# Performance work log

Measured on AMD Instinct MI355X. Metric: run time of the kernel, lower is better.

Reference implementation:

```python
import jax, jax.numpy as jnp
import numpy as np
from jax import lax

B, C, T = 512, 63, 250          # batch, EEG channels, timepoints
S = 10                           # number of subjects
E = 4                            # emb_size of CNN projection
HID, PROJ = 184, 1024            # hidden_dim (=4*46), embed_dim
EPS = 1e-5
DN = ('NCHW', 'OIHW', 'NCHW')


def setup_inputs() -> dict:
    key = jax.random.key(0)
    ks = jax.random.split(key, 16)
    p = {}
    p['x'] = jax.random.normal(ks[0], (B, C, T), dtype=jnp.float32)
    p['subjects'] = jax.random.randint(ks[1], (B,), 0, S, dtype=jnp.int32)
    # per-subject Linear(T, T): weight [S, T, T], bias [S, T]
    p['W_subj'] = jax.random.normal(ks[2], (S, T, T), dtype=jnp.float32) * 0.02
    p['b_subj'] = jnp.zeros((S, T), dtype=jnp.float32)
    # tsconv
    p['conv1_w'] = jax.random.normal(ks[3], (40, 1, 1, 5), dtype=jnp.float32) * 0.1
    p['conv1_b'] = jnp.zeros((40,), dtype=jnp.float32)
    p['bn1_g'] = jnp.ones((40,), dtype=jnp.float32)
    p['bn1_b'] = jnp.zeros((40,), dtype=jnp.float32)
    p['conv2_w'] = jax.random.normal(ks[4], (40, 40, C, 1), dtype=jnp.float32) * 0.02
    p['conv2_b'] = jnp.zeros((40,), dtype=jnp.float32)
    p['bn2_g'] = jnp.ones((40,), dtype=jnp.float32)
    p['bn2_b'] = jnp.zeros((40,), dtype=jnp.float32)
    # 1x1 projection conv to emb_size
    p['proj_w'] = jax.random.normal(ks[5], (E, 40, 1, 1), dtype=jnp.float32) * 0.1
    p['proj_b'] = jnp.zeros((E,), dtype=jnp.float32)
    # MLP projector
    p['fc1_w'] = jax.random.normal(ks[6], (PROJ, HID), dtype=jnp.float32) * 0.05
    p['fc1_b'] = jnp.zeros((PROJ,), dtype=jnp.float32)
    p['fc2_w'] = jax.random.normal(ks[7], (PROJ, PROJ), dtype=jnp.float32) * 0.02
    p['fc2_b'] = jnp.zeros((PROJ,), dtype=jnp.float32)
    p['ln_g'] = jnp.ones((PROJ,), dtype=jnp.float32)
    p['ln_b'] = jnp.zeros((PROJ,), dtype=jnp.float32)
    return p


def _bn(h, g, b):
    # BatchNorm2d with batch statistics over (N, H, W), NCHW layout
    mu = jnp.mean(h, axis=(0, 2, 3), keepdims=True)
    var = jnp.var(h, axis=(0, 2, 3), keepdims=True)
    return (h - mu) * lax.rsqrt(var + EPS) * g[None, :, None, None] + b[None, :, None, None]


def _avgpool_w(h, k, s):
    # average pool over last (W) dim, kernel k stride s
    summed = lax.reduce_window(h, 0.0, lax.add, (1, 1, 1, k), (1, 1, 1, s), 'VALID')
    return summed / k


def reference(x, subjects, W_subj, b_subj, conv1_w, conv1_b, bn1_g, bn1_b,
              conv2_w, conv2_b, bn2_g, bn2_b, proj_w, proj_b,
              fc1_w, fc1_b, fc2_w, fc2_b, ln_g, ln_b):
    # --- subject-conditioned linear dispatch (grouped GEMM via gather) ---
    Wg = W_subj[subjects]                      # [B, T, T]
    bg = b_subj[subjects]                      # [B, T]
    x_eeg = jnp.einsum('bct,bst->bcs', x, Wg) + bg[:, None, :]   # [B, C, T]

    # --- Spatio_Temporal_CNN ---
    h = x_eeg[:, None, :, :]                   # [B, 1, C, T]
    h = lax.conv_general_dilated(h, conv1_w, (1, 1), 'VALID', dimension_numbers=DN)
    h = h + conv1_b[None, :, None, None]       # [B, 40, C, 246]
    h = _avgpool_w(h, 17, 5)                   # [B, 40, C, 46]
    h = jax.nn.elu(_bn(h, bn1_g, bn1_b))
    h = lax.conv_general_dilated(h, conv2_w, (1, 1), 'VALID', dimension_numbers=DN)
    h = h + conv2_b[None, :, None, None]       # [B, 40, 1, 46]
    h = jax.nn.elu(_bn(h, bn2_g, bn2_b))       # dropout = identity (eval)
    h = lax.conv_general_dilated(h, proj_w, (1, 1), 'VALID', dimension_numbers=DN)
    h = h + proj_b[None, :, None, None]        # [B, E, 1, 46]
    # Rearrange 'b e h w -> b (h w) e' then flatten -> [B, 46*E] = [B, 184]
    z = jnp.transpose(h, (0, 2, 3, 1)).reshape(h.shape[0], -1)

    # --- MLP projector ---
    h1 = z @ fc1_w.T + fc1_b                   # [B, 1024]
    r = jax.nn.gelu(h1, approximate=False) @ fc2_w.T + fc2_b
    h2 = h1 + r                                # ResidualAdd (dropout = identity)
    mu = jnp.mean(h2, axis=-1, keepdims=True)
    var = jnp.var(h2, axis=-1, keepdims=True)
    return (h2 - mu) * lax.rsqrt(var + EPS) * ln_g + ln_b
```

## Files before the change

### kernel.cpp

```cpp
#include <hip/hip_runtime.h>
#include <hip/hip_bf16.h>

#define K2 2520
#define PROJ 1024
#define HID 184
#define N1F (512.f*63.f*46.f)
#define N2F (512.f*46.f)

typedef float f32x4 __attribute__((ext_vector_type(4)));
typedef short bf16x8 __attribute__((ext_vector_type(8)));
typedef unsigned short u16;
typedef unsigned short ushort8 __attribute__((ext_vector_type(8)));
typedef unsigned int u32;
typedef unsigned int u32x4 __attribute__((ext_vector_type(4)));

__device__ __forceinline__ u16 f2bf(float f) {
    unsigned u = __builtin_bit_cast(unsigned, f);
    return (u16)((u + 0x7FFFu + ((u >> 16) & 1u)) >> 16);
}
__device__ __forceinline__ float bf2f(u16 h) {
    unsigned u = ((unsigned)h) << 16;
    return __builtin_bit_cast(float, u);
}
__device__ __forceinline__ u32 cvtpk(float lo, float hi) {
    u32 r;
    asm("v_cvt_pk_bf16_f32 %0, %1, %2" : "=v"(r) : "v"(lo), "v"(hi));
    return r;
}

__global__ void kX(const float* __restrict__ W, const float* __restrict__ w2,
                   const float* __restrict__ fw1, const float* __restrict__ fw2,
                   u16* __restrict__ Wbf, u16* __restrict__ Wbf2,
                   u16* __restrict__ fwbf1, u16* __restrict__ fwbf2, float* stats) {
    int bid = blockIdx.x, tid = threadIdx.x;
    if (bid == 0 && tid < 320) stats[tid] = 0.f;
    if (bid < 2560) {
        int i = bid*256 + tid;
        int j  = i & 7, kg = (i >> 3) & 3, row = (i >> 5) & 15;
        int nf = (i >> 9) & 15, ks = (i >> 13) & 7, sj = i >> 16;
        int s_ = nf*16 + row, t_ = ks*32 + kg*8 + j;
        float v = (s_ < 250 && t_ < 250) ? W[(size_t)sj*62500 + s_*250 + t_] : 0.f;
        Wbf[i] = f2bf(v);
    } else if (bid < 3034) {
        int i = (bid-2560)*256 + tid;
        int n = i / 2528, k = i - n*2528;
        float v = 0.f;
        if (n < 40 && k < K2) { int c = k/40, o = k - c*40; v = w2[n*K2 + o*63 + c]; }
        Wbf2[i] = f2bf(v);
    } else if (bid < 3802) {
        int i = (bid-3034)*256 + tid;
        int n = i/192, k = i - n*192;
        fwbf1[i] = f2bf(k < HID ? fw1[n*HID + k] : 0.f);
    } else {
        int i = (bid-3802)*256 + tid;
        fwbf2[i] = f2bf(fw2[i]);
    }
}

#define XS(c,s) xs[(c)*258 + (s)]
__global__ __launch_bounds__(256) void kAB(const float* __restrict__ x,
                                           const int* __restrict__ subj,
                                           const u16* __restrict__ Wpk,
                                           const float* __restrict__ bsub,
                                           const float* __restrict__ w1,
                                           const float* __restrict__ b1,
                                           u16* __restrict__ pooled,
                                           float* __restrict__ stats) {
    __shared__ float xs[32*258 + 16];
    __shared__ u16 effh[48*32] __attribute__((aligned(16)));
    __shared__ u16 effl[48*32] __attribute__((aligned(16)));
    __shared__ float biasL[256];
    __shared__ float sS[4][48], sQ[4][48];
    int b = blockIdx.x, ch = blockIdx.y;
    int sj = subj[b];
    int tid = threadIdx.x;
    int wv = tid >> 6, lane = tid & 63, row = lane & 15, kg = lane >> 4;

    {
        int srow = tid >> 3, st8 = tid & 7;
        int cg0 = ch*32 + srow;
        const float* xrow = x + ((size_t)b*63 + (cg0 < 63 ? cg0 : 62))*250;
        #pragma unroll
        for (int q = 0; q < 16; ++q) {
            int c2i = st8 + 8*q;
            if (c2i < 125) {
                float2 v = *(const float2*)&xrow[2*c2i];
                *(float2*)&XS(srow, 2*c2i) = v;
            }
        }
        XS(srow, 250 + st8) = 0.f;
        if (tid < 16) xs[32*258 + tid] = 0.f;
    }
    biasL[tid] = (tid < 250) ? bsub[sj*250 + tid] : 0.f;
    for (int i = tid; i < 1536; i += 256) {
        int o = i >> 5, tap = i & 31;
        float e = 0.f;
        if (o < 40 && tap < 21) {
            #pragma unroll
            for (int k = 0; k < 5; ++k) { int u = tap - k; if (u >= 0 && u <= 16) e += w1[o*5+k]; }
            e *= (1.f/17.f);
        }
        u16 h = f2bf(e);
        effh[i] = h;
        effl[i] = f2bf(e - bf2f(h));
    }
    __syncthreads();

    int cgrp = wv & 1, nfh = wv >> 1;
    const u16* Wp = Wpk + (size_t)sj*65536 + ((size_t)row*4 + kg)*8;
    f32x4 acc[8];
    #pragma unroll
    for (int i = 0; i < 8; ++i) acc[i] = (f32x4){0.f,0.f,0.f,0.f};
    #pragma unroll
    for (int ks = 0; ks < 8; ++ks) {
        int tb = ks*32 + kg*8;
        float av[8];
        #pragma unroll
        for (int j = 0; j < 8; ++j) av[j] = XS(cgrp*16 + row, tb + j);
        u32x4 p;
        p[0]=cvtpk(av[0],av[1]); p[1]=cvtpk(av[2],av[3]);
        p[2]=cvtpk(av[4],av[5]); p[3]=cvtpk(av[6],av[7]);
        bf16x8 af = __builtin_bit_cast(bf16x8, p);
        #pragma unroll
        for (int nf2 = 0; nf2 < 8; ++nf2) {
            bf16x8 bv = *(const bf16x8*)(Wp + (size_t)(ks*16 + nfh*8 + nf2)*512);
            acc[nf2] = __builtin_amdgcn_mfma_f32_16x16x32_bf16(af, bv, acc[nf2], 0, 0, 0);
        }
    }
    __syncthreads();
    int cw = cgrp*16 + kg*4;
    #pragma unroll
    for (int nf2 = 0; nf2 < 8; ++nf2) {
        int s = (nfh*8 + nf2)*16 + row;
        float bias = biasL[s];
        #pragma unroll
        for (int r = 0; r < 4; ++r) XS(cw + r, s) = acc[nf2][r] + bias;
    }
    __syncthreads();

    bf16x8 bvh[3], bvl[3];
    float b1v[3];
    bool ovalid[3];
    #pragma unroll
    for (int nt = 0; nt < 3; ++nt) {
        bvh[nt] = *(const bf16x8*)(effh + (nt*16 + row)*32 + kg*8);
        bvl[nt] = *(const bf16x8*)(effl + (nt*16 + row)*32 + kg*8);
        int o = nt*16 + row;
        ovalid[nt] = o < 40;
        b1v[nt] = ovalid[nt] ? b1[o] : 0.f;
    }
    float ss[3] = {0.f,0.f,0.f}, sq[3] = {0.f,0.f,0.f};
    int climit = ch ? 31 : 32;
    for (int c2 = wv; c2 < climit; c2 += 4) {
        f32x4 acc2[3][3];
        #pragma unroll
        for (int mt = 0; mt < 3; ++mt) {
            int base = c2*258 + 5*(mt*16 + row) + kg*8;
            float av[8];
            #pragma unroll
            for (int j = 0; j < 8; ++j) av[j] = xs[base + j];
            u32x4 ph, pl;
            #pragma unroll
            for (int p = 0; p < 4; ++p) {
                u32 h = cvtpk(av[2*p], av[2*p+1]);
                float h0 = __builtin_bit_cast(float, h << 16);
                float h1 = __builtin_bit_cast(float, h & 0xFFFF0000u);
                ph[p] = h;
                pl[p] = cvtpk(av[2*p] - h0, av[2*p+1] - h1);
            }
            bf16x8 afh = __builtin_bit_cast(bf16x8, ph);
            bf16x8 afl = __builtin_bit_cast(bf16x8, pl);
            #pragma unroll
            for (int nt = 0; nt < 3; ++nt) {
                f32x4 a = (f32x4){b1v[nt], b1v[nt], b1v[nt], b1v[nt]};
                a = __builtin_amdgcn_mfma_f32_16x16x32_bf16(afl, bvh[nt], a, 0, 0, 0);
                a = __builtin_amdgcn_mfma_f32_16x16x32_bf16(afh, bvl[nt], a, 0, 0, 0);
                a = __builtin_amdgcn_mfma_f32_16x16x32_bf16(afh, bvh[nt], a, 0, 0, 0);
                acc2[mt][nt] = a;
            }
        }
        u16* prow = pooled + (size_t)b*46*K2 + (ch*32 + c2)*40;
        #pragma unroll
        for (int mt = 0; mt < 3; ++mt) {
            #pragma unroll
            for (int nt = 0; nt < 3; ++nt) {
                if (!ovalid[nt]) continue;
                int o = nt*16 + row;
                #pragma unroll
                for (int r = 0; r < 4; ++r) {
                    int w = mt*16 + kg*4 + r;
                    if (mt < 2 || w < 46) {
                        float v = acc2[mt][nt][r];
                        prow[(size_t)w*K2 + o] = f2bf(v);
                        ss[nt] += v;
                        sq[nt] = fmaf(v, v, sq[nt]);
                    }
                }
            }
        }
    }
    #pragma unroll
    for (int nt = 0; nt < 3; ++nt) {
        float s = ss[nt], q = sq[nt];
        s += __shfl_xor(s, 16); q += __shfl_xor(q, 16);
        s += __shfl_xor(s, 32); q += __shfl_xor(q, 32);
        if (kg == 0) { sS[wv][nt*16 + row] = s; sQ[wv][nt*16 + row] = q; }
    }
    __syncthreads();
    if (tid < 40) {
        float s = sS[0][tid]+sS[1][tid]+sS[2][tid]+sS[3][tid];
        float q = sQ[0][tid]+sQ[1][tid]+sQ[2][tid]+sQ[3][tid];
        atomicAdd(&stats[tid], s);
        atomicAdd(&stats[40 + tid], q);
    }
}

__global__ __launch_bounds__(256) void kD(const u16* __restrict__ pooled,
                                          const u16* __restrict__ Wbf2,
                                          const float* __restrict__ b2,
                                          const float* __restrict__ g1,
                                          const float* __restrict__ bb1,
                                          const float* __restrict__ stats,
                                          float* __restrict__ out2,
                                          float* __restrict__ statw) {
    __shared__ float2 scsh[40];
    __shared__ float mrg[2][64][12];
    __shared__ float redS[2][48], redQ[2][48];
    int tid = threadIdx.x;
    if (tid < 40) {
        float mean = stats[tid] / N1F;
        float var  = stats[40 + tid] / N1F - mean * mean;
        float sc   = g1[tid] * rsqrtf(var + 1e-5f);
        scsh[tid] = make_float2(sc, bb1[tid] - mean * sc);
    }
    __syncthreads();
    int wv = tid >> 6, lane = tid & 63, row = lane & 15, kg = lane >> 4;
    int rowgrp = wv >> 1, khalf = wv & 1;
    int mbase = blockIdx.x*32 + rowgrp*16;
    const u16* pr = pooled + (size_t)(mbase + row) * K2;
    f32x4 acc[3];
    #pragma unroll
    for (int i = 0; i < 3; ++i) acc[i] = (f32x4){0.f,0.f,0.f,0.f};

    int ksBeg = khalf ? 39 : 0, ksEnd = khalf ? 79 : 39;
    for (int ks = ksBeg; ks < ksEnd; ++ks) {
        int kbase = ks*32 + kg*8;
        ushort8 cur = *(const ushort8*)&pr[kbase];
        bf16x8 bv0 = *(const bf16x8*)(Wbf2 + (size_t)(row     )*2528 + kbase);
        bf16x8 bv1 = *(const bf16x8*)(Wbf2 + (size_t)(16 + row)*2528 + kbase);
        bf16x8 bv2 = *(const bf16x8*)(Wbf2 + (size_t)(32 + row)*2528 + kbase);
        bf16x8 af;
        bool valid = (ks < 78) | (kg < 3);
        if (valid) {
            int m5 = 4*ks + kg;
            int o0 = (m5 - 5*((m5*52429) >> 18)) * 8;
            #pragma unroll
            for (int j = 0; j < 8; ++j) {
                float2 sshf = scsh[o0 + j];
                float a = fmaf(bf2f(cur[j]), sshf.x, sshf.y);
                float e = a > 0.f ? a : __expf(a) - 1.f;
                af[j] = (short)f2bf(e);
            }
        } else {
            #pragma unroll
            for (int j = 0; j < 8; ++j) af[j] = 0;
        }
        acc[0] = __builtin_amdgcn_mfma_f32_16x16x32_bf16(af, bv0, acc[0], 0, 0, 0);
        acc[1] = __builtin_amdgcn_mfma_f32_16x16x32_bf16(af, bv1, acc[1], 0, 0, 0);
        acc[2] = __builtin_amdgcn_mfma_f32_16x16x32_bf16(af, bv2, acc[2], 0, 0, 0);
    }

    if (khalf) {
        #pragma unroll
        for (int nf = 0; nf < 3; ++nf)
            #pragma unroll
            for (int r = 0; r < 4; ++r) mrg[rowgrp][lane][nf*4 + r] = acc[nf][r];
    }
    __syncthreads();
    if (!khalf) {
        float sN[3] = {0.f,0.f,0.f}, qN[3] = {0.f,0.f,0.f};
        #pragma unroll
        for (int nf = 0; nf < 3; ++nf) {
            int n = nf*16 + row;
            #pragma unroll
            for (int r = 0; r < 4; ++r) acc[nf][r] += mrg[rowgrp][lane][nf*4 + r];
            if (n < 40) {
                float bias = b2[n];
                #pragma unroll
                for (int r = 0; r < 4; ++r) {
                    float v = acc[nf][r] + bias;
                    out2[(size_t)(mbase + kg*4 + r)*40 + n] = v;
                    sN[nf] += v; qN[nf] += v*v;
                }
            }
        }
        #pragma unroll
        for (int nf = 0; nf < 3; ++nf) {
            float s = sN[nf], q = qN[nf];
            s += __shfl_xor(s, 16); q += __shfl_xor(q, 16);
            s += __shfl_xor(s, 32); q += __shfl_xor(q, 32);
            if (kg == 0) { redS[rowgrp][nf*16 + row] = s; redQ[rowgrp][nf*16 + row] = q; }
        }
    }
    __syncthreads();
    if (tid < 40) {
        atomicAdd(&statw[160 + tid], redS[0][tid] + redS[1][tid]);
        atomicAdd(&statw[200 + tid], redQ[0][tid] + redQ[1][tid]);
    }
}

__global__ void kF(const float* __restrict__ out2, const float* __restrict__ stats,
                   const float* __restrict__ g2, const float* __restrict__ bb2,
                   const float* __restrict__ pw, const float* __restrict__ pb,
                   u16* __restrict__ zbf) {
    int b = blockIdx.x, t = threadIdx.x;
    __shared__ float sc[40], sh[40], pws[160];
    __shared__ float o2[1840];
    if (t < 40) {
        float mean = stats[160 + t] / N2F;
        float var  = stats[200 + t] / N2F - mean * mean;
        float s    = g2[t] * rsqrtf(var + 1e-5f);
        sc[t] = s;
        sh[t] = bb2[t] - mean * s;
    }
    if (t < 160) pws[t] = pw[t];
    for (int i = t; i < 1840; i += 256) o2[i] = out2[(size_t)b*1840 + i];
    __syncthreads();
    if (t < 192) {
        float accv = 0.f;
        if (t < HID) {
            int w = t >> 2, e = t & 3;
            accv = pb[e];
            for (int o = 0; o < 40; ++o) {
                float a = o2[w*40 + o];
                float act = a * sc[o] + sh[o];
                act = act > 0.f ? act : __expf(act) - 1.f;
                accv = fmaf(act, pws[e*40 + o], accv);
            }
        }
        zbf[(size_t)b*192 + t] = f2bf(accv);
    }
}

__global__ __launch_bounds__(256) void kG1(const u16* __restrict__ zbf, const u16* __restrict__ fwbf1,
                                           const float* __restrict__ fb,
                                           float* __restrict__ h1, u16* __restrict__ gbf) {
    int n0 = blockIdx.x * 64, m0 = blockIdx.y * 16;
    int tid = threadIdx.x, wv = tid >> 6, lane = tid & 63, row = lane & 15, kg = lane >> 4;
    const u16* zr = zbf + (size_t)(m0 + row) * 192;
    const u16* wr = fwbf1 + (size_t)(n0 + wv*16 + row) * 192;
    f32x4 acc = (f32x4){0.f,0.f,0.f,0.f};
    #pragma unroll
    for (int ks = 0; ks < 6; ++ks) {
        bf16x8 av = *(const bf16x8*)(zr + ks*32 + kg*8);
        bf16x8 bv = *(const bf16x8*)(wr + ks*32 + kg*8);
        acc = __builtin_amdgcn_mfma_f32_16x16x32_bf16(av, bv, acc, 0, 0, 0);
    }
    int n = n0 + wv*16 + row;
    float bias = fb[n];
    #pragma unroll
    for (int r = 0; r < 4; ++r) {
        int m = m0 + kg*4 + r;
        float v = acc[r] + bias;
        h1[(size_t)m*PROJ + n] = v;
        float ge = 0.5f * v * (1.f + erff(v * 0.70710678118f));
        gbf[(size_t)m*PROJ + n] = f2bf(ge);
    }
}

__global__ __launch_bounds__(256) void kG2(const u16* __restrict__ gbf, const u16* __restrict__ fwbf,
                                           const float* __restrict__ fb, const float* __restrict__ h1,
                                           float* __restrict__ h2) {
    int n0 = blockIdx.x * 32, m0 = blockIdx.y * 64;
    int tid = threadIdx.x;
    int wv = tid >> 6, lane = tid & 63, row = lane & 15, kg = lane >> 4;
    const u16* gr = gbf + (size_t)(m0 + wv*16 + row) * PROJ;
    f32x4 acc[2];
    #pragma unroll
    for (int i = 0; i < 2; ++i) acc[i] = (f32x4){0.f,0.f,0.f,0.f};
    for (int ks = 0; ks < 32; ++ks) {
        int kbase = ks*32 + kg*8;
        bf16x8 av  = *(const bf16x8*)(gr + kbase);
        bf16x8 bv0 = *(const bf16x8*)(fwbf + (size_t)(n0      + row)*PROJ + kbase);
        bf16x8 bv1 = *(const bf16x8*)(fwbf + (size_t)(n0 + 16 + row)*PROJ + kbase);
        acc[0] = __builtin_amdgcn_mfma_f32_16x16x32_bf16(av, bv0, acc[0], 0, 0, 0);
        acc[1] = __builtin_amdgcn_mfma_f32_16x16x32_bf16(av, bv1, acc[1], 0, 0, 0);
    }
    int m = m0 + wv*16 + kg*4;
    #pragma unroll
    for (int nf = 0; nf < 2; ++nf) {
        int n = n0 + nf*16 + row;
        float bias = fb[n];
        #pragma unroll
        for (int r = 0; r < 4; ++r)
            h2[(size_t)(m + r)*PROJ + n] = acc[nf][r] + bias + h1[(size_t)(m + r)*PROJ + n];
    }
}

__global__ __launch_bounds__(256) void kG3(const float* __restrict__ h2, const float* __restrict__ lg,
                                           const float* __restrict__ lb, float* __restrict__ out) {
    int b = blockIdx.x, tid = threadIdx.x;
    float4 v = *(const float4*)&h2[(size_t)b*PROJ + tid*4];
    float s = v.x + v.y + v.z + v.w;
    float q = v.x*v.x + v.y*v.y + v.z*v.z + v.w*v.w;
    __shared__ float ps[4], pq[4], mb[2];
    int wave = tid >> 6, lane = tid & 63;
    #pragma unroll
    for (int d = 32; d >= 1; d >>= 1) { s += __shfl_down(s, d); q += __shfl_down(q, d); }
    if (lane == 0) { ps[wave] = s; pq[wave] = q; }
    __syncthreads();
    if (tid == 0) {
        float S = ps[0]+ps[1]+ps[2]+ps[3], Q = pq[0]+pq[1]+pq[2]+pq[3];
        float mean = S / 1024.f, var = Q / 1024.f - mean*mean;
        mb[0] = mean; mb[1] = rsqrtf(var + 1e-5f);
    }
    __syncthreads();
    float mean = mb[0], inv = mb[1];
    float4 g4 = *(const float4*)&lg[tid*4];
    float4 b4 = *(const float4*)&lb[tid*4];
    float4 o4;
    o4.x = (v.x - mean)*inv*g4.x + b4.x;
    o4.y = (v.y - mean)*inv*g4.y + b4.y;
    o4.z = (v.z - mean)*inv*g4.z + b4.z;
    o4.w = (v.w - mean)*inv*g4.w + b4.w;
    *(float4*)&out[(size_t)b*PROJ + tid*4] = o4;
}

extern "C" void kernel_launch(void* const* d_in, const int* in_sizes, int n_in,
                              void* d_out, int out_size, void* d_ws, size_t ws_size,
                              hipStream_t stream) {
    const float* x       = (const float*)d_in[0];
    const int*   subjects= (const int*)  d_in[1];
    const float* W_subj  = (const float*)d_in[2];
    const float* b_subj  = (const float*)d_in[3];
    const float* conv1_w = (const float*)d_in[4];
    const float* conv1_b = (const float*)d_in[5];
    const float* bn1_g   = (const float*)d_in[6];
    const float* bn1_b   = (const float*)d_in[7];
    const float* conv2_w = (const float*)d_in[8];
    const float* conv2_b = (const float*)d_in[9];
    const float* bn2_g   = (const float*)d_in[10];
    const float* bn2_b   = (const float*)d_in[11];
    const float* proj_w  = (const float*)d_in[12];
    const float* proj_b  = (const float*)d_in[13];
    const float* fc1_w   = (const float*)d_in[14];
    const float* fc1_b   = (const float*)d_in[15];
    const float* fc2_w   = (const float*)d_in[16];
    const float* fc2_b   = (const float*)d_in[17];
    const float* ln_g    = (const float*)d_in[18];
    const float* ln_b    = (const float*)d_in[19];
    float* out = (float*)d_out;

    char* ws = (char*)d_ws;
    u16*   pooled = (u16*)  ws;
    float* out2   = (float*)(ws + 118702144);
    u16*   zbf    = (u16*)  (ws + 122470464);
    float* h1     = (float*)(ws + 122667072);
    float* h2     = (float*)(ws + 124764224);
    u16*   gbf    = (u16*)  (ws + 126861376);
    float* stats  = (float*)(ws + 127909952);
    u16*   Wbf    = (u16*)  (ws + 127914048);
    u16*   Wbf2   = (u16*)  (ws + 129224768);
    u16*   fwbf2  = (u16*)  (ws + 129467456);
    u16*   fwbf1  = (u16*)  (ws + 131564608);

    kX  <<<7898, 256, 0, stream>>>(W_subj, conv2_w, fc1_w, fc2_w, Wbf, Wbf2, fwbf1, fwbf2, stats);
    kAB <<<dim3(512, 2), 256, 0, stream>>>(x, subjects, Wbf, b_subj, conv1_w, conv1_b, pooled, stats);
    kD  <<<736, 256, 0, stream>>>(pooled, Wbf2, conv2_b, bn1_g, bn1_b, stats, out2, stats);
    kF  <<<512, 256, 0, stream>>>(out2, stats, bn2_g, bn2_b, proj_w, proj_b, zbf);
    kG1 <<<dim3(16, 32), 256, 0, stream>>>(zbf, fwbf1, fc1_b, h1, gbf);
    kG2 <<<dim3(32, 8), 256, 0, stream>>>(gbf, fwbf2, fc2_b, h1, h2);
    kG3 <<<512, 256, 0, stream>>>(h2, ln_g, ln_b, out);
    (void)in_sizes; (void)n_in; (void)out_size; (void)ws_size;
}
```

Before: 261.8 us.

## Transpose pooled-activation layout and swap MFMA operands for packed coalesced stores

The conv1/pool kernel now swaps the MFMA A/B operands so each lane holds four consecutive output channels, which lets it write packed 8-byte bf16 stores into a new [b][c][w][o] pooled layout instead of scattered 2-byte stores strided by K2. BN statistics are reduced per channel-quad with shuffles across rows. The consumer GEMM kernel computes addresses for the new layout and software-prefetches the next activation vector one iteration ahead. Reads in kD become strided by channel blocks rather than contiguous, which may hurt its load efficiency.

```diff
diff --git a/kernel.cpp b/kernel.cpp
--- a/kernel.cpp
+++ b/kernel.cpp
@@ -12,6 +12,7 @@
 typedef unsigned short u16;
 typedef unsigned short ushort8 __attribute__((ext_vector_type(8)));
 typedef unsigned int u32;
+typedef unsigned int u32x2 __attribute__((ext_vector_type(2)));
 typedef unsigned int u32x4 __attribute__((ext_vector_type(4)));
 
 __device__ __forceinline__ u16 f2bf(float f) {
@@ -138,21 +139,20 @@
     }
     __syncthreads();
 
-    bf16x8 bvh[3], bvl[3];
-    float b1v[3];
-    bool ovalid[3];
+    bf16x8 avh[3], avl[3];
+    f32x4 cin3[3];
     #pragma unroll
     for (int nt = 0; nt < 3; ++nt) {
-        bvh[nt] = *(const bf16x8*)(effh + (nt*16 + row)*32 + kg*8);
-        bvl[nt] = *(const bf16x8*)(effl + (nt*16 + row)*32 + kg*8);
-        int o = nt*16 + row;
-        ovalid[nt] = o < 40;
-        b1v[nt] = ovalid[nt] ? b1[o] : 0.f;
-    }
-    float ss[3] = {0.f,0.f,0.f}, sq[3] = {0.f,0.f,0.f};
+        avh[nt] = *(const bf16x8*)(effh + (nt*16 + row)*32 + kg*8);
+        avl[nt] = *(const bf16x8*)(effl + (nt*16 + row)*32 + kg*8);
+        int ob = nt*16 + kg*4;
+        if (ob < 40) cin3[nt] = *(const f32x4*)&b1[ob];
+        else         cin3[nt] = (f32x4){0.f,0.f,0.f,0.f};
+    }
+    float ss[3][4] = {}, sq[3][4] = {};
     int climit = ch ? 31 : 32;
     for (int c2 = wv; c2 < climit; c2 += 4) {
-        f32x4 acc2[3][3];
+        u16* prow = pooled + (size_t)b*115920 + (size_t)(ch*32 + c2)*1840;
         #pragma unroll
         for (int mt = 0; mt < 3; ++mt) {
             int base = c2*258 + 5*(mt*16 + row) + kg*8;
@@ -168,32 +168,26 @@
                 ph[p] = h;
                 pl[p] = cvtpk(av[2*p] - h0, av[2*p+1] - h1);
             }
-            bf16x8 afh = __builtin_bit_cast(bf16x8, ph);
-            bf16x8 afl = __builtin_bit_cast(bf16x8, pl);
+            bf16x8 bfh = __builtin_bit_cast(bf16x8, ph);
+            bf16x8 bfl = __builtin_bit_cast(bf16x8, pl);
+            int w = mt*16 + row;
+            bool wvalid = w < 46;
             #pragma unroll
             for (int nt = 0; nt < 3; ++nt) {
-                f32x4 a = (f32x4){b1v[nt], b1v[nt], b1v[nt], b1v[nt]};
-                a = __builtin_amdgcn_mfma_f32_16x16x32_bf16(afl, bvh[nt], a, 0, 0, 0);
-                a = __builtin_amdgcn_mfma_f32_16x16x32_bf16(afh, bvl[nt], a, 0, 0, 0);
-                a = __builtin_amdgcn_mfma_f32_16x16x32_bf16(afh, bvh[nt], a, 0, 0, 0);
-                acc2[mt][nt] = a;
-            }
-        }
-        u16* prow = pooled + (size_t)b*46*K2 + (ch*32 + c2)*40;
-        #pragma unroll
-        for (int mt = 0; mt < 3; ++mt) {
-            #pragma unroll
-            for (int nt = 0; nt < 3; ++nt) {
-                if (!ovalid[nt]) continue;
-                int o = nt*16 + row;
-                #pragma unroll
-                for (int r = 0; r < 4; ++r) {
-                    int w = mt*16 + kg*4 + r;
-                    if (mt < 2 || w < 46) {
-                        float v = acc2[mt][nt][r];
-                        prow[(size_t)w*K2 + o] = f2bf(v);
-                        ss[nt] += v;
-                        sq[nt] = fmaf(v, v, sq[nt]);
+                f32x4 a = cin3[nt];
+                a = __builtin_amdgcn_mfma_f32_16x16x32_bf16(avh[nt], bfl, a, 0, 0, 0);
+                a = __builtin_amdgcn_mfma_f32_16x16x32_bf16(avl[nt], bfh, a, 0, 0, 0);
+                a = __builtin_amdgcn_mfma_f32_16x16x32_bf16(avh[nt], bfh, a, 0, 0, 0);
+                int ob = nt*16 + kg*4;
+                if (wvalid && ob < 40) {
+                    u32x2 pk;
+                    pk[0] = cvtpk(a[0], a[1]);
+                    pk[1] = cvtpk(a[2], a[3]);
+                    *(u32x2*)&prow[(size_t)w*40 + ob] = pk;
+                    #pragma unroll
+                    for (int r = 0; r < 4; ++r) {
+                        ss[nt][r] += a[r];
+                        sq[nt][r] = fmaf(a[r], a[r], sq[nt][r]);
                     }
                 }
             }
@@ -201,10 +195,18 @@
     }
     #pragma unroll
     for (int nt = 0; nt < 3; ++nt) {
-        float s = ss[nt], q = sq[nt];
-        s += __shfl_xor(s, 16); q += __shfl_xor(q, 16);
-        s += __shfl_xor(s, 32); q += __shfl_xor(q, 32);
-        if (kg == 0) { sS[wv][nt*16 + row] = s; sQ[wv][nt*16 + row] = q; }
+        #pragma unroll
+        for (int r = 0; r < 4; ++r) {
+            float s = ss[nt][r], q = sq[nt][r];
+            s += __shfl_xor(s, 1); q += __shfl_xor(q, 1);
+            s += __shfl_xor(s, 2); q += __shfl_xor(q, 2);
+            s += __shfl_xor(s, 4); q += __shfl_xor(q, 4);
+            s += __shfl_xor(s, 8); q += __shfl_xor(q, 8);
+            if (row == 0) {
+                int ob = nt*16 + kg*4;
+                if (ob < 40) { sS[wv][ob + r] = s; sQ[wv][ob + r] = q; }
+            }
+        }
     }
     __syncthreads();
     if (tid < 40) {
@@ -237,23 +239,34 @@
     int wv = tid >> 6, lane = tid & 63, row = lane & 15, kg = lane >> 4;
     int rowgrp = wv >> 1, khalf = wv & 1;
     int mbase = blockIdx.x*32 + rowgrp*16;
-    const u16* pr = pooled + (size_t)(mbase + row) * K2;
+    int m = mbase + row;
+    int bb = m / 46, ww = m - bb*46;
+    const u16* prl = pooled + (size_t)bb*115920 + (size_t)ww*40;
     f32x4 acc[3];
     #pragma unroll
     for (int i = 0; i < 3; ++i) acc[i] = (f32x4){0.f,0.f,0.f,0.f};
 
     int ksBeg = khalf ? 39 : 0, ksEnd = khalf ? 79 : 39;
+    int t0 = 4*ksBeg + kg;
+    int ci = (t0*52429) >> 18, o5i = t0 - 5*ci;
+    ushort8 cur = *(const ushort8*)(prl + ci*1840 + o5i*8);
     for (int ks = ksBeg; ks < ksEnd; ++ks) {
+        ushort8 nxt = cur;
+        if (ks + 1 < ksEnd) {
+            int tn = 4*(ks+1) + kg;
+            int cn = (tn*52429) >> 18, o5n = tn - 5*cn;
+            nxt = *(const ushort8*)(prl + cn*1840 + o5n*8);
+        }
         int kbase = ks*32 + kg*8;
-        ushort8 cur = *(const ushort8*)&pr[kbase];
         bf16x8 bv0 = *(const bf16x8*)(Wbf2 + (size_t)(row     )*2528 + kbase);
         bf16x8 bv1 = *(const bf16x8*)(Wbf2 + (size_t)(16 + row)*2528 + kbase);
         bf16x8 bv2 = *(const bf16x8*)(Wbf2 + (size_t)(32 + row)*2528 + kbase);
         bf16x8 af;
         bool valid = (ks < 78) | (kg < 3);
         if (valid) {
-            int m5 = 4*ks + kg;
-            int o0 = (m5 - 5*((m5*52429) >> 18)) * 8;
+            int tt = 4*ks + kg;
+            int cc = (tt*52429) >> 18;
+            int o0 = (tt - 5*cc) * 8;
             #pragma unroll
             for (int j = 0; j < 8; ++j) {
                 float2 sshf = scsh[o0 + j];
@@ -268,6 +281,7 @@
         acc[0] = __builtin_amdgcn_mfma_f32_16x16x32_bf16(af, bv0, acc[0], 0, 0, 0);
         acc[1] = __builtin_amdgcn_mfma_f32_16x16x32_bf16(af, bv1, acc[1], 0, 0, 0);
         acc[2] = __builtin_amdgcn_mfma_f32_16x16x32_bf16(af, bv2, acc[2], 0, 0, 0);
+        cur = nxt;
     }
 
     if (khalf) {
```

Result: faster. 254.0 us (-3.0%).
